# Performance work log

Measured on AMD Instinct MI355X. Metric: run time of the kernel, lower is better.

## Reference

```python
import jax, jax.numpy as jnp
import numpy as np

HIDDEN = 64

def setup_inputs() -> dict:
    key = jax.random.key(0)
    ks = jax.random.split(key, 7)
    B, T, I, H, O = 4096, 512, 28, 64, 10
    s_ih = 1.0 / np.sqrt(H)
    return {
        "x": jax.random.normal(ks[0], (B, T, I), dtype=jnp.float32),
        "W_ih": jax.random.uniform(ks[1], (H, I), jnp.float32, -s_ih, s_ih),
        "W_hh": jax.random.uniform(ks[2], (H, H), jnp.float32, -s_ih, s_ih),
        "b_ih": jax.random.uniform(ks[3], (H,), jnp.float32, -s_ih, s_ih),
        "b_hh": jax.random.uniform(ks[4], (H,), jnp.float32, -s_ih, s_ih),
        "W_out": jax.random.uniform(ks[5], (O, H), jnp.float32, -s_ih, s_ih),
        "b_out": jax.random.uniform(ks[6], (O,), jnp.float32, -s_ih, s_ih),
    }

def reference(x, W_ih, W_hh, b_ih, b_hh, W_out, b_out):
    B, T, I = x.shape
    # Precompute input contributions for all timesteps: [T, B, H]
    xW = jnp.einsum('bti,hi->tbh', x, W_ih) + b_ih + b_hh
    h0 = jnp.zeros((B, HIDDEN), dtype=x.dtype)

    def step(h, xw_t):
        h_new = jnp.tanh(xw_t + h @ W_hh.T)
        return h_new, None

    h_last, _ = jax.lax.scan(step, h0, xW)
    return h_last @ W_out.T + b_out
```

## Files before the change

### kernel.cpp

```cpp
#include <hip/hip_runtime.h>


#define T_STEPS 512
#define I_DIM   28
#define H_DIM   64
#define O_DIM   10
#define ROWS    16
#define LDSS    68
#define HBUF    (ROWS * LDSS)

typedef __attribute__((ext_vector_type(8))) short bfrag;
typedef __attribute__((ext_vector_type(4))) float ffrag;
typedef __attribute__((ext_vector_type(4))) float float4v;

#define MFMA(a,b,c) __builtin_amdgcn_mfma_f32_16x16x32_bf16((a),(b),(c),0,0,0)
#define LDS_BARRIER() asm volatile("s_waitcnt lgkmcnt(0)\n\ts_barrier" ::: "memory")

union FragU { bfrag s; unsigned u[4]; };

__device__ __forceinline__ unsigned hi_pack(float f0, float f1){
  return __builtin_amdgcn_perm(__float_as_uint(f1), __float_as_uint(f0), 0x07060302u);
}

__device__ __forceinline__ void split8v(float4v a, float4v b, bfrag& hi, bfrag& lo){
  float f[8] = {a.x,a.y,a.z,a.w, b.x,b.y,b.z,b.w};
  FragU H, L;
#pragma unroll
  for (int m = 0; m < 4; m++){
    float f0 = f[2*m], f1 = f[2*m+1];
    H.u[m] = hi_pack(f0, f1);
    float l0 = f0 - __uint_as_float(__float_as_uint(f0) & 0xffff0000u);
    float l1 = f1 - __uint_as_float(__float_as_uint(f1) & 0xffff0000u);
    L.u[m] = hi_pack(l0, l1);
  }
  hi = H.s; lo = L.s;
}

__device__ __forceinline__ float fast_tanh(float p){
  float e = __builtin_amdgcn_exp2f(p * 2.88539008177792681f);
  return __builtin_fmaf(-2.0f, __builtin_amdgcn_rcpf(e + 1.0f), 1.0f);
}

#define BODY(T_C, XA, XB, BUF_OFF)                                             \
  {                                                                            \
    bfrag xhi, xlo;                                                            \
    split8v(XA, XB, xhi, xlo);                                                 \
    {                                                                          \
      int tload = (T_C) + 4; if (tload > T_STEPS - 1) tload = T_STEPS - 1;     \
      const float* lp = xrow + (size_t)tload * I_DIM;                          \
      XA = *(const float4v*)lp;                                                \
      XB = *(const float4v*)(qlt3 ? lp + 4 : lp);                              \
    }                                                                          \
    ffrag acA, acB;                                                            \
            \
    acA = MFMA(xhi, wih_hi, biasf);                                            \
    acB = MFMA(xhi, wih_lo, zfrag);                                            \
    acA = MFMA(xlo, wih_hi, acA);                                              \
                             \
    acA = MFMA(h_hi[0], whh_hi[0], acA);                                       \
    acB = MFMA(h_hi[1], whh_hi[1], acB);                                       \
    acA = MFMA(h_lo[0], whh_hi[0], acA);                                       \
    acB = MFMA(h_lo[1], whh_hi[1], acB);                                       \
    acA = MFMA(h_hi[0], whh_lo[0], acA);                                       \
    acB = MFMA(h_hi[1], whh_lo[1], acB);                                       \
                \
    float* wb = hTb + (BUF_OFF) + (q*4)*LDSS + c + 16*w;                       \
    wb[0*LDSS] = fast_tanh(acA.x + acB.x);                                     \
    wb[1*LDSS] = fast_tanh(acA.y + acB.y);                                     \
    wb[2*LDSS] = fast_tanh(acA.z + acB.z);                                     \
    wb[3*LDSS] = fast_tanh(acA.w + acB.w);                                     \
    LDS_BARRIER();                                                             \
      \
    const float* rb = hTb + (BUF_OFF) + c*LDSS + q*8;                          \
    split8v(*(const float4v*)rb,        *(const float4v*)(rb + 4),             \
            h_hi[0], h_lo[0]);                                                 \
    split8v(*(const float4v*)(rb + 32), *(const float4v*)(rb + 36),            \
            h_hi[1], h_lo[1]);                                                 \
  }

__global__ __launch_bounds__(256, 1) void rnn_fused(
    const float* __restrict__ x,
    const float* __restrict__ W_ih,
    const float* __restrict__ W_hh,
    const float* __restrict__ b_ih,
    const float* __restrict__ b_hh,
    const float* __restrict__ W_out,
    const float* __restrict__ b_out,
    float* __restrict__ out)
{
  __shared__ float hTb[2 * HBUF];
  const int tid  = threadIdx.x;
  const int w    = tid >> 6;
  const int lane = tid & 63;
  const int c    = lane & 15;
  const int q    = lane >> 4;
  const bool qlt3 = (q < 3);
  const int rowbase = blockIdx.x * ROWS;

  bfrag whh_hi[2], whh_lo[2];
#pragma unroll
  for (int kt = 0; kt < 2; ++kt){
    const float* p = W_hh + (c + 16*w)*H_DIM + kt*32 + q*8;
    split8v(*(const float4v*)p, *(const float4v*)(p + 4), whh_hi[kt], whh_lo[kt]);
  }

  bfrag wih_hi, wih_lo;
  {
    const float* p = W_ih + (c + 16*w)*I_DIM + q*8;
    float4v a = *(const float4v*)p;
    float4v b;
    if (qlt3) b = *(const float4v*)(p + 4);
    else      b = (float4v){0.f, 0.f, 0.f, 0.f};
    split8v(a, b, wih_hi, wih_lo);
  }

  ffrag biasf;
  {
    float bb = b_ih[c + 16*w] + b_hh[c + 16*w];
    biasf.x = bb; biasf.y = bb; biasf.z = bb; biasf.w = bb;
  }
  const ffrag zfrag = {0.f, 0.f, 0.f, 0.f};

  bfrag h_hi[2], h_lo[2];
  {
    FragU Z; Z.u[0]=Z.u[1]=Z.u[2]=Z.u[3]=0;
    h_hi[0] = Z.s; h_lo[0] = Z.s; h_hi[1] = Z.s; h_lo[1] = Z.s;
  }

  const float* xrow = x + ((size_t)(rowbase + c) * T_STEPS) * I_DIM + q*8;
  float4v xa[4], xb[4];
#pragma unroll
  for (int s = 0; s < 4; ++s){
    const float* p = xrow + (size_t)s * I_DIM;
    xa[s] = *(const float4v*)p;
    xb[s] = *(const float4v*)(qlt3 ? p + 4 : p);
  }

#pragma unroll 1
  for (int tb = 0; tb < T_STEPS; tb += 4){
    BODY(tb + 0, xa[0], xb[0], HBUF);
    BODY(tb + 1, xa[1], xb[1], 0);
    BODY(tb + 2, xa[2], xb[2], HBUF);
    BODY(tb + 3, xa[3], xb[3], 0);
  }

  if (w == 0){
    for (int oo = q; oo < O_DIM; oo += 4){
      float s = b_out[oo];
#pragma unroll 8
      for (int k = 0; k < H_DIM; ++k)
        s += hTb[c*LDSS + k] * W_out[oo*H_DIM + k];
      out[(size_t)(rowbase + c)*O_DIM + oo] = s;
    }
  }
}

extern "C" void kernel_launch(void* const* d_in, const int* in_sizes, int n_in,
                              void* d_out, int out_size, void* d_ws, size_t ws_size,
                              hipStream_t stream) {
  const float* x     = (const float*)d_in[0];
  const float* W_ih  = (const float*)d_in[1];
  const float* W_hh  = (const float*)d_in[2];
  const float* b_ih  = (const float*)d_in[3];
  const float* b_hh  = (const float*)d_in[4];
  const float* W_out = (const float*)d_in[5];
  const float* b_out = (const float*)d_in[6];
  float* out = (float*)d_out;

  int B = in_sizes[0] / (T_STEPS * I_DIM);
  rnn_fused<<<B / ROWS, 256, 0, stream>>>(x, W_ih, W_hh, b_ih, b_hh, W_out, b_out, out);
}
```

Before: 459.7 us.

## Store hidden state as pre-split bf16 hi/lo in LDS and halve rows per block

```diff
diff --git a/kernel.cpp b/kernel.cpp
--- a/kernel.cpp
+++ b/kernel.cpp
@@ -5,9 +5,9 @@
 #define I_DIM   28
 #define H_DIM   64
 #define O_DIM   10
-#define ROWS    16
-#define LDSS    68
-#define HBUF    (ROWS * LDSS)
+#define ROWS    8
+#define HSTR    72
+#define HELE    (16 * HSTR)
 
 typedef __attribute__((ext_vector_type(8))) short bfrag;
 typedef __attribute__((ext_vector_type(4))) float ffrag;
@@ -63,19 +63,27 @@
     acB = MFMA(h_lo[1], whh_hi[1], acB);                                       \
     acA = MFMA(h_hi[0], whh_lo[0], acA);                                       \
     acB = MFMA(h_hi[1], whh_lo[1], acB);                                       \
-                \
-    float* wb = hTb + (BUF_OFF) + (q*4)*LDSS + c + 16*w;                       \
-    wb[0*LDSS] = fast_tanh(acA.x + acB.x);                                     \
-    wb[1*LDSS] = fast_tanh(acA.y + acB.y);                                     \
-    wb[2*LDSS] = fast_tanh(acA.z + acB.z);                                     \
-    wb[3*LDSS] = fast_tanh(acA.w + acB.w);                                     \
+          \
+    float fv[4];                                                               \
+    fv[0] = fast_tanh(acA.x + acB.x);                                          \
+    fv[1] = fast_tanh(acA.y + acB.y);                                          \
+    fv[2] = fast_tanh(acA.z + acB.z);                                          \
+    fv[3] = fast_tanh(acA.w + acB.w);                                          \
+    short* wH = hHi + (BUF_OFF) + (q*4)*HSTR + (c + 16*w);                     \
+    short* wL = hLo + (BUF_OFF) + (q*4)*HSTR + (c + 16*w);                     \
+    _Pragma("unroll")                                                          \
+    for (int e = 0; e < 4; ++e){                                               \
+      unsigned u = __float_as_uint(fv[e]);                                     \
+      wH[e*HSTR] = (short)(u >> 16);                                           \
+      float rem = fv[e] - __uint_as_float(u & 0xffff0000u);                    \
+      wL[e*HSTR] = (short)(__float_as_uint(rem) >> 16);                        \
+    }                                                                          \
     LDS_BARRIER();                                                             \
-      \
-    const float* rb = hTb + (BUF_OFF) + c*LDSS + q*8;                          \
-    split8v(*(const float4v*)rb,        *(const float4v*)(rb + 4),             \
-            h_hi[0], h_lo[0]);                                                 \
-    split8v(*(const float4v*)(rb + 32), *(const float4v*)(rb + 36),            \
-            h_hi[1], h_lo[1]);                                                 \
+           \
+    const short* rH = hHi + (BUF_OFF) + c*HSTR + q*8;                          \
+    const short* rL = hLo + (BUF_OFF) + c*HSTR + q*8;                          \
+    h_hi[0] = *(const bfrag*)rH;  h_hi[1] = *(const bfrag*)(rH + 32);          \
+    h_lo[0] = *(const bfrag*)rL;  h_lo[1] = *(const bfrag*)(rL + 32);          \
   }
 
 __global__ __launch_bounds__(256, 1) void rnn_fused(
@@ -86,9 +94,11 @@
     const float* __restrict__ b_hh,
     const float* __restrict__ W_out,
     const float* __restrict__ b_out,
-    float* __restrict__ out)
+    float* __restrict__ out,
+    int Btot)
 {
-  __shared__ float hTb[2 * HBUF];
+  __shared__ __attribute__((aligned(16))) short hHi[2 * HELE];
+  __shared__ __attribute__((aligned(16))) short hLo[2 * HELE];
   const int tid  = threadIdx.x;
   const int w    = tid >> 6;
   const int lane = tid & 63;
@@ -127,7 +137,8 @@
     h_hi[0] = Z.s; h_lo[0] = Z.s; h_hi[1] = Z.s; h_lo[1] = Z.s;
   }
 
-  const float* xrow = x + ((size_t)(rowbase + c) * T_STEPS) * I_DIM + q*8;
+  int xr = rowbase + c; if (xr > Btot - 1) xr = Btot - 1;
+  const float* xrow = x + ((size_t)xr * T_STEPS) * I_DIM + q*8;
   float4v xa[4], xb[4];
 #pragma unroll
   for (int s = 0; s < 4; ++s){
@@ -138,18 +149,21 @@
 
 #pragma unroll 1
   for (int tb = 0; tb < T_STEPS; tb += 4){
-    BODY(tb + 0, xa[0], xb[0], HBUF);
+    BODY(tb + 0, xa[0], xb[0], HELE);
     BODY(tb + 1, xa[1], xb[1], 0);
-    BODY(tb + 2, xa[2], xb[2], HBUF);
+    BODY(tb + 2, xa[2], xb[2], HELE);
     BODY(tb + 3, xa[3], xb[3], 0);
   }
 
-  if (w == 0){
+  if (w == 0 && c < ROWS){
     for (int oo = q; oo < O_DIM; oo += 4){
       float s = b_out[oo];
 #pragma unroll 8
-      for (int k = 0; k < H_DIM; ++k)
-        s += hTb[c*LDSS + k] * W_out[oo*H_DIM + k];
+      for (int k = 0; k < H_DIM; ++k){
+        float hv = __uint_as_float(((unsigned)(unsigned short)hHi[c*HSTR + k]) << 16)
+                 + __uint_as_float(((unsigned)(unsigned short)hLo[c*HSTR + k]) << 16);
+        s += hv * W_out[oo*H_DIM + k];
+      }
       out[(size_t)(rowbase + c)*O_DIM + oo] = s;
     }
   }
@@ -168,5 +182,5 @@
   float* out = (float*)d_out;
 
   int B = in_sizes[0] / (T_STEPS * I_DIM);
-  rnn_fused<<<B / ROWS, 256, 0, stream>>>(x, W_ih, W_hh, b_ih, b_hh, W_out, b_out, out);
+  rnn_fused<<<B / ROWS, 256, 0, stream>>>(x, W_ih, W_hh, b_ih, b_hh, W_out, b_out, out, B);
 }
```

Measured after the change: 518.2 us. +12.7%, slower.
